# Kernel tuning notes

Measured on AMD Instinct MI355X. Metric: run time of the kernel, lower is better.

The kernel has to match this reference:

```python
import jax, jax.numpy as jnp
import numpy as np
import math

B, L, NV, PRED = 8, 512, 32, 96
D, PL, STRIDE = 128, 16, 8
E, TOPN, H = 8, 2, 512
P = (L - PL) // STRIDE + 2  # 64 patches (includes replication pad of STRIDE)
BAL_COEF, Z_COEF = 0.01, 0.001


def sinusoid_pe(n, d):
    pos = np.arange(n, dtype=np.float32)[:, None]
    div = np.exp(np.arange(0, d, 2, dtype=np.float32) * -(math.log(10000.0) / d))
    pe = np.zeros((n, d), dtype=np.float32)
    pe[:, 0::2] = np.sin(pos * div)
    pe[:, 1::2] = np.cos(pos * div)
    return jnp.asarray(pe)


def setup_inputs() -> dict:
    key = jax.random.key(0)
    ks = jax.random.split(key, 10)
    return {
        "x_enc": jax.random.normal(ks[0], (B, L, NV), jnp.float32),
        "x_mark_enc": jax.random.normal(ks[1], (B, L, 4), jnp.float32),
        "x_dec": jnp.zeros((B, 144, NV), jnp.float32),
        "x_mark_dec": jnp.zeros((B, 144, 4), jnp.float32),
        "W_patch": jax.random.normal(ks[2], (PL, D), jnp.float32) * 0.05,
        "Wg": jax.random.normal(ks[3], (D, E), jnp.float32) * 0.05,
        "W1": jax.random.normal(ks[4], (E, D, H), jnp.float32) * 0.05,
        "b1": jnp.zeros((E, H), jnp.float32),
        "W2": jax.random.normal(ks[5], (E, H, D), jnp.float32) * 0.05,
        "b2": jnp.zeros((E, D), jnp.float32),
        "W_head": jax.random.normal(ks[6], (D * P, PRED), jnp.float32) * 0.02,
        "b_head": jnp.zeros((PRED,), jnp.float32),
    }


def _forward(x_enc, W_patch, Wg, W1, b1, W2, b2, W_head, b_head):
    # instance norm over time (detached stats, like the torch code)
    means = jax.lax.stop_gradient(jnp.mean(x_enc, axis=1, keepdims=True))
    xc = x_enc - means
    stdev = jax.lax.stop_gradient(
        jnp.sqrt(jnp.mean((x_enc - means) ** 2, axis=1, keepdims=True) + 1e-5))
    xc = xc / stdev
    # [B, NV, L] -> replication pad right by STRIDE -> unfold into patches
    x = jnp.transpose(xc, (0, 2, 1))
    xp = jnp.pad(x, ((0, 0), (0, 0), (0, STRIDE)), mode="edge")
    idx = jnp.arange(P)[:, None] * STRIDE + jnp.arange(PL)[None, :]  # [P, PL]
    patches = xp[:, :, idx]  # [B, NV, P, PL]
    tok = patches.reshape(B * NV, P, PL)
    h = jnp.einsum("tpl,ld->tpd", tok, W_patch) + sinusoid_pe(P, D)[None]
    # ---- MoE over flattened tokens ----
    N = B * NV * P
    xf = h.reshape(N, D)
    logits = xf @ Wg                              # [N, E]
    probs = jax.nn.softmax(logits, axis=-1)
    gates, tops = jax.lax.top_k(probs, TOPN)      # [N, TOPN]
    # dense per-expert FFN (exact GELU, as nn.GELU default)
    eh = jax.nn.gelu(jnp.einsum("nd,edh->neh", xf, W1) + b1, approximate=False)
    eo = jnp.einsum("neh,ehd->ned", eh, W2) + b2  # [N, E, D]
    onehot = jax.nn.one_hot(tops, E, dtype=xf.dtype)          # [N, TOPN, E]
    cw = jnp.einsum("nk,nke->ne", gates, onehot)              # combine weights
    y = jnp.einsum("ne,ned->nd", cw, eo)
    # aux losses: load-balance + router z-loss
    mask = onehot.sum(axis=1)                                  # [N, E]
    balance = E * jnp.sum(jnp.mean(probs, axis=0) * jnp.mean(mask, axis=0)) / TOPN
    zloss = jnp.mean(jax.nn.logsumexp(logits, axis=-1) ** 2)
    aux = BAL_COEF * balance + Z_COEF * zloss
    # ---- head ----
    enc = y.reshape(B, NV, P, D).transpose(0, 1, 3, 2)         # [B, NV, D, P]
    flat = enc.reshape(B, NV, D * P)
    dec = flat @ W_head + b_head                               # [B, NV, PRED]
    dec = jnp.transpose(dec, (0, 2, 1))                        # [B, PRED, NV]
    dec = dec * stdev[:, 0, :][:, None, :] + means[:, 0, :][:, None, :]
    return dec, aux


def reference(x_enc, x_mark_enc, x_dec, x_mark_dec, W_patch, Wg, W1, b1, W2, b2,
              W_head, b_head):
    return _forward(x_enc, W_patch, Wg, W1, b1, W2, b2, W_head, b_head)
```

## Files before the change

kernel.cpp:

```cpp
#include <hip/hip_runtime.h>
#include <math.h>


typedef __attribute__((ext_vector_type(8))) short bf16x8;
typedef __attribute__((ext_vector_type(4))) float f32x4;

__device__ __forceinline__ float bf2f(unsigned short u){
  unsigned x = ((unsigned)u) << 16; float f; __builtin_memcpy(&f, &x, 4); return f;
}
__device__ __forceinline__ unsigned short f2bf(float f){
  unsigned x; __builtin_memcpy(&x, &f, 4);
  return (unsigned short)((x + 0x7FFFu + ((x >> 16) & 1u)) >> 16);
}
__device__ __forceinline__ float ldin(const void* p, int i, int f32){
  return f32 ? ((const float*)p)[i] : bf2f(((const unsigned short*)p)[i]);
}
__device__ __forceinline__ void stout(void* p, int i, float v, int f32){
  if (f32) ((float*)p)[i] = v; else ((unsigned short*)p)[i] = f2bf(v);
}
__device__ __forceinline__ f32x4 mfma16(bf16x8 a, bf16x8 b, f32x4 c){
  return __builtin_amdgcn_mfma_f32_16x16x32_bf16(a, b, c, 0, 0, 0);
}
#define BAR_RAW() asm volatile("s_waitcnt lgkmcnt(0)\n\ts_barrier" ::: "memory")
__device__ __forceinline__ float gelu_fast(float v){
  float u = v*v;
  float inner = v * fmaf(0.044715f, u, 1.0f);
  float e = __expf(-1.5957691216f * inner);
  return v / (1.0f + e);
}

#define OFF_SUMS   64
#define OFF_MEANS  256
#define OFF_STDS   1280
#define OFF_ECNT   2304
#define OFF_PE     3328
#define OFF_W1T    134400
#define OFF_W2T    1182976
#define OFF_WHT    2231552
#define OFF_CW     3804416
#define OFF_XFBF   4328704
#define OFF_FLATB  8523008
#define OFF_EO     12717312
#define OFF_TOKSLOT 79826176
#define OFF_DECP   79957248

__global__ __launch_bounds__(256) void k_prep_tr(const void* __restrict__ W1,
                                                 const void* __restrict__ W2,
                                                 const void* __restrict__ Wh,
                                                 int f32, float* pe,
                                                 unsigned short* W1T, unsigned short* W2T,
                                                 unsigned short* WhT){
  int t = threadIdx.x;
  if (blockIdx.x == 0){
    for (int i = t; i < 8192; i += 256){
      int p = i >> 7, d = i & 127;
      float freq = __expf(-(float)(d & ~1) * 0.07195578415606394f);
      float ang = (float)p * freq;
      pe[i] = (d & 1) ? __cosf(ang) : __sinf(ang);
    }
    return;
  }
  __shared__ float tile[32*33];
  int tb = blockIdx.x - 1;
  int r = t >> 3, cg = (t & 7) * 4;
  const void* src; unsigned short* dst;
  int in0, instride, out0, outstride;
  if (tb < 512){
    int e = tb >> 6, ti = tb & 63, d0 = (ti & 3) * 32, h0 = (ti >> 2) * 32;
    src = W1; dst = W1T;
    in0 = e*65536 + d0*512 + h0; instride = 512;
    out0 = e*65536 + h0*128 + d0; outstride = 128;
  } else if (tb < 1024){
    int tc = tb - 512;
    int e = tc >> 6, ti = tc & 63, d0 = (ti & 3) * 32, h0 = (ti >> 2) * 32;
    src = W2; dst = W2T;
    in0 = e*65536 + h0*128 + d0; instride = 128;
    out0 = e*65536 + d0*512 + h0; outstride = 512;
  } else {
    int tc = tb - 1024;
    int kt = tc / 3, nt = tc - kt*3;
    int k0 = kt*32, n0 = nt*32;
    src = Wh; dst = WhT;
    in0 = k0*96 + n0; instride = 96;
    out0 = n0*8192 + k0; outstride = 8192;
  }
  #pragma unroll
  for (int j = 0; j < 4; ++j)
    tile[r*33 + cg + j] = ldin(src, in0 + r*instride + cg + j, f32);
  __syncthreads();
  ushort4 o;
  o.x = f2bf(tile[(cg+0)*33 + r]);
  o.y = f2bf(tile[(cg+1)*33 + r]);
  o.z = f2bf(tile[(cg+2)*33 + r]);
  o.w = f2bf(tile[(cg+3)*33 + r]);
  *(ushort4*)(dst + out0 + r*outstride + cg) = o;
}

__global__ __launch_bounds__(256) void k_embed(const void* __restrict__ xe,
                                               const void* __restrict__ Wp,
                                               const void* __restrict__ Wg,
                                               int f32,
                                               const float* __restrict__ peg,
                                               float* means, float* stds,
                                               unsigned short* xfbf, float* cwg,
                                               float* sums,
                                               int* ecnt, int* elist, int* tokslot){
  __shared__ float xn[512];
  __shared__ float WpL[2048];
  __shared__ float WgL[1024];
  __shared__ float Xf[8192];
  __shared__ float lp[1024];
  __shared__ float taux[576];
  __shared__ float reds[256], redss[256];
  __shared__ float msh[2];
  __shared__ int lcnt[8], lbase[8];

  int bv = blockIdx.x;
  int b = bv >> 5, v = bv & 31;
  int t = threadIdx.x;

  if (t < 8) lcnt[t] = 0;

  float x0 = ldin(xe, (b*512 + t)*32 + v, f32);
  float x1 = ldin(xe, (b*512 + t + 256)*32 + v, f32);
  xn[t] = x0; xn[t+256] = x1;
  reds[t] = x0 + x1; redss[t] = x0*x0 + x1*x1;
  #pragma unroll
  for (int it = 0; it < 8; ++it)
    WpL[it*256 + t] = ldin(Wp, it*256 + t, f32);
  #pragma unroll
  for (int j = 0; j < 4; ++j)
    WgL[j*256 + t] = ldin(Wg, j*256 + t, f32);
  __syncthreads();
  for (int s = 128; s > 0; s >>= 1){
    if (t < s){ reds[t] += reds[t+s]; redss[t] += redss[t+s]; }
    __syncthreads();
  }
  if (t == 0){
    float m = reds[0] / 512.f;
    float sd = sqrtf(redss[0] / 512.f - m*m + 1e-5f);
    msh[0] = m; msh[1] = 1.f / sd;
    means[bv] = m; stds[bv] = sd;
  }
  __syncthreads();
  float mean = msh[0], rstd = msh[1];
  xn[t] = (xn[t] - mean) * rstd;
  xn[t+256] = (xn[t+256] - mean) * rstd;
  __syncthreads();
  {
    int p = t >> 2, q = t & 3;
    float tv[16];
    #pragma unroll
    for (int l = 0; l < 16; ++l){
      int xi = p*8 + l; if (xi > 511) xi = 511;
      tv[l] = xn[xi];
    }
    for (int dd = 0; dd < 32; ++dd){
      int d = q*32 + dd;
      float acc = peg[p*128 + d];
      #pragma unroll
      for (int l = 0; l < 16; ++l) acc += tv[l] * WpL[l*128 + d];
      Xf[p*128 + d] = acc;
    }
  }
  __syncthreads();
  if (t < 128){
    int p = t >> 1, half = t & 1;
    float s[8] = {0,0,0,0,0,0,0,0};
    for (int d = half*64; d < half*64 + 64; ++d){
      float xv = Xf[p*128 + d];
      #pragma unroll
      for (int e = 0; e < 8; ++e) s[e] += xv * WgL[d*8 + e];
    }
    #pragma unroll
    for (int e = 0; e < 8; ++e) lp[(p*2 + half)*8 + e] = s[e];
  }
  __syncthreads();
  int bi = 0, si = 0, lo0 = 0, lo1 = 0;
  if (t < 64){
    int p = t;
    float lg[8];
    #pragma unroll
    for (int e = 0; e < 8; ++e) lg[e] = lp[(p*2)*8 + e] + lp[(p*2+1)*8 + e];
    float m = lg[0];
    #pragma unroll
    for (int e = 1; e < 8; ++e) m = fmaxf(m, lg[e]);
    float pr[8]; float se = 0.f;
    #pragma unroll
    for (int e = 0; e < 8; ++e){ pr[e] = __expf(lg[e] - m); se += pr[e]; }
    float inv = 1.f / se;
    float lse = m + logf(se);
    #pragma unroll
    for (int e = 0; e < 8; ++e) pr[e] *= inv;
    float best = -1.f;
    #pragma unroll
    for (int e = 0; e < 8; ++e) if (pr[e] > best){ best = pr[e]; bi = e; }
    float sec = -1.f;
    #pragma unroll
    for (int e = 0; e < 8; ++e) if (e != bi && pr[e] > sec){ sec = pr[e]; si = e; }
    #pragma unroll
    for (int e = 0; e < 8; ++e){
      float w = (e == bi) ? best : ((e == si) ? sec : 0.f);
      cwg[(bv*64 + p)*8 + e] = w;
      taux[p*9 + e] = pr[e];
    }
    taux[p*9 + 8] = lse * lse;
    lp[p] = (float)bi; lp[64 + p] = (float)si;
    lo0 = atomicAdd(&lcnt[bi], 1);
    lo1 = atomicAdd(&lcnt[si], 1);
  }
  __syncthreads();
  if (t < 8) lbase[t] = atomicAdd(ecnt + t*32, lcnt[t]);
  __syncthreads();
  if (t < 64){
    int n = bv*64 + t;
    int p0 = lbase[bi] + lo0, p1 = lbase[si] + lo1;
    elist[bi*16384 + p0] = n;
    elist[si*16384 + p1] = n;
    tokslot[n*2]     = (bi << 14) + p0;
    tokslot[n*2 + 1] = (si << 14) + p1;
  }
  if (t < 17){
    float s = 0.f;
    if (t < 8){ for (int p = 0; p < 64; ++p) s += taux[p*9 + t]; }
    else if (t < 16){
      int e = t - 8;
      for (int p = 0; p < 64; ++p)
        s += ((int)lp[p] == e || (int)lp[64+p] == e) ? 1.f : 0.f;
    }
    else { for (int p = 0; p < 64; ++p) s += taux[p*9 + 8]; }
    atomicAdd(sums + t, s);
  }
  #pragma unroll
  for (int pass = 0; pass < 4; ++pass){
    int idx = pass*256 + t;
    int base = idx*8;
    bf16x8 o;
    #pragma unroll
    for (int j = 0; j < 8; ++j) o[j] = (short)f2bf(Xf[base + j]);
    *(bf16x8*)(xfbf + bv*8192 + base) = o;
  }
}

__global__ __launch_bounds__(256, 3) void k_moe(const unsigned short* __restrict__ xfbf,
                                                const unsigned short* __restrict__ W1T,
                                                const unsigned short* __restrict__ W2T,
                                                const void* __restrict__ b1g,
                                                int f32,
                                                const float* __restrict__ cwg,
                                                const int* __restrict__ ecnt,
                                                const int* __restrict__ elist,
                                                float* __restrict__ Eo){
  __shared__ __align__(16) char lds[49664];
  short* Xs  = (short*)(lds);
  short* Bu1 = (short*)(lds + 8704);
  short* Bu2 = (short*)(lds + 26112);
  short* Ag  = (short*)(lds + 44544);
  float* cws = (float*)(lds + 49152);
  int*   lsn = (int*)(lds + 49280);

  int t = threadIdx.x;
  int wave = t >> 6, lane = t & 63;
  int quad = lane >> 4, li = lane & 15;
  int c1 = wave * 16;
  int c2 = wave * 32;

  for (int tb = blockIdx.x; tb < 1536; tb += 768){
    int e = 8, ti = 0;
    {
      int acc = 0;
      #pragma unroll
      for (int ee = 0; ee < 8; ++ee){
        int tl = (ecnt[ee*32] + 31) >> 5;
        if (e == 8 && tb < acc + tl){ e = ee; ti = tb - acc; }
        acc += tl;
      }
    }
    if (e == 8) break;
    int cntE = ecnt[e*32];
    int tbase = ti*32;

    const unsigned short* W1e = W1T + e*65536;
    const unsigned short* W2e = W2T + e*65536;

    bf16x8 pf1[4], pf2[4];
    #pragma unroll
    for (int pass = 0; pass < 4; ++pass){
      int idx = pass*64 + lane;
      int row = idx >> 4, kg = idx & 15;
      pf1[pass] = *(const bf16x8*)(W1e + (c1 + row)*128 + kg*8);
    }
    #pragma unroll
    for (int pass = 0; pass < 4; ++pass){
      int idx = pass*64 + lane;
      int row = idx >> 3, kg = idx & 7;
      pf2[pass] = *(const bf16x8*)(W2e + (c2 + row)*512 + kg*8);
    }

    if (t < 32){
      int ok = (tbase + t) < cntE;
      int n = ok ? elist[e*16384 + tbase + t] : 0;
      lsn[t] = n;
      cws[t] = ok ? cwg[n*8 + e] : 0.f;
    }
    __syncthreads();
    #pragma unroll
    for (int pass = 0; pass < 2; ++pass){
      int idx = pass*256 + t;
      int row = idx >> 4, kg = idx & 15;
      int n = lsn[row];
      *(bf16x8*)(Xs + row*136 + kg*8) =
        *(const bf16x8*)(xfbf + n*128 + kg*8);
    }
    float cwv[2][4];
    #pragma unroll
    for (int rt = 0; rt < 2; ++rt)
      #pragma unroll
      for (int r = 0; r < 4; ++r)
        cwv[rt][r] = cws[rt*16 + quad*4 + r];
    __syncthreads();

    f32x4 Yacc[2][2];
    #pragma unroll
    for (int a = 0; a < 2; ++a)
      #pragma unroll
      for (int bb = 0; bb < 2; ++bb){ f32x4 z = {0.f,0.f,0.f,0.f}; Yacc[a][bb] = z; }

    for (int hc = 0; hc < 8; ++hc){
      #pragma unroll
      for (int pass = 0; pass < 4; ++pass){
        int idx = pass*64 + lane;
        int row = idx >> 4, kg = idx & 15;
        *(bf16x8*)(Bu1 + (c1 + row)*136 + kg*8) = pf1[pass];
      }
      #pragma unroll
      for (int pass = 0; pass < 4; ++pass){
        int idx = pass*64 + lane;
        int row = idx >> 3, kg = idx & 7;
        *(bf16x8*)(Bu2 + (c2 + row)*72 + kg*8) = pf2[pass];
      }
      float bias = ldin(b1g, e*512 + hc*64 + c1 + li, f32);
      if (hc < 7){
        #pragma unroll
        for (int pass = 0; pass < 4; ++pass){
          int idx = pass*64 + lane;
          int row = idx >> 4, kg = idx & 15;
          pf1[pass] = *(const bf16x8*)(W1e + ((hc+1)*64 + c1 + row)*128 + kg*8);
        }
        #pragma unroll
        for (int pass = 0; pass < 4; ++pass){
          int idx = pass*64 + lane;
          int row = idx >> 3, kg = idx & 7;
          pf2[pass] = *(const bf16x8*)(W2e + (c2 + row)*512 + (hc+1)*64 + kg*8);
        }
      }
      f32x4 acc1[2];
      { f32x4 z = {0.f,0.f,0.f,0.f}; acc1[0] = z; acc1[1] = z; }
      #pragma unroll
      for (int ks = 0; ks < 4; ++ks){
        int kk = ks*32 + quad*8;
        bf16x8 a0 = *(const bf16x8*)(Xs + li*136 + kk);
        bf16x8 a1 = *(const bf16x8*)(Xs + (16 + li)*136 + kk);
        bf16x8 b0 = *(const bf16x8*)(Bu1 + (c1 + li)*136 + kk);
        acc1[0] = mfma16(a0, b0, acc1[0]);
        acc1[1] = mfma16(a1, b0, acc1[1]);
      }
      BAR_RAW();
      #pragma unroll
      for (int rt = 0; rt < 2; ++rt){
        #pragma unroll
        for (int r = 0; r < 4; ++r){
          int row = rt*16 + quad*4 + r;
          float g = gelu_fast(acc1[rt][r] + bias);
          Ag[row*72 + c1 + li] = (short)f2bf(g * cwv[rt][r]);
        }
      }
      BAR_RAW();
      #pragma unroll
      for (int ks = 0; ks < 2; ++ks){
        int kk = ks*32 + quad*8;
        bf16x8 a0 = *(const bf16x8*)(Ag + li*72 + kk);
        bf16x8 a1 = *(const bf16x8*)(Ag + (16 + li)*72 + kk);
        #pragma unroll
        for (int ct = 0; ct < 2; ++ct){
          bf16x8 bb = *(const bf16x8*)(Bu2 + (c2 + ct*16 + li)*72 + kk);
          Yacc[0][ct] = mfma16(a0, bb, Yacc[0][ct]);
          Yacc[1][ct] = mfma16(a1, bb, Yacc[1][ct]);
        }
      }
    }
    #pragma unroll
    for (int ct = 0; ct < 2; ++ct){
      int col = c2 + ct*16 + li;
      #pragma unroll
      for (int rt = 0; rt < 2; ++rt)
        #pragma unroll
        for (int r = 0; r < 4; ++r){
          int row = rt*16 + quad*4 + r;
          if (tbase + row < cntE)
            Eo[(size_t)((e << 14) + tbase + row)*128 + col] = Yacc[rt][ct][r];
        }
    }
  }
}

__global__ __launch_bounds__(256) void k_flat(const float* __restrict__ Eo,
                                              const int* __restrict__ tokslot,
                                              const float* __restrict__ cwg,
                                              const void* __restrict__ b2g,
                                              int f32,
                                              unsigned short* __restrict__ flatb){
  __shared__ float Yl[64*130];
  __shared__ float b2f[1024];
  __shared__ float cwl[512];
  __shared__ int tsl[128];
  int bv = blockIdx.x;
  int t = threadIdx.x;
  if (t < 64){
    int2 v = *(const int2*)(tokslot + (bv*64 + t)*2);
    tsl[t*2] = v.x; tsl[t*2+1] = v.y;
  }
  #pragma unroll
  for (int j = 0; j < 4; ++j) b2f[j*256 + t] = ldin(b2g, j*256 + t, f32);
  #pragma unroll
  for (int j = 0; j < 2; ++j) cwl[j*256 + t] = cwg[bv*512 + j*256 + t];
  __syncthreads();
  #pragma unroll
  for (int pass = 0; pass < 32; ++pass){
    int idx = pass*256 + t;
    int row = idx >> 7, col = idx & 127;
    Yl[row*130 + col] = Eo[(size_t)tsl[row*2]*128 + col]
                      + Eo[(size_t)tsl[row*2+1]*128 + col];
  }
  __syncthreads();
  int d = t >> 1, ph = (t & 1) * 32;
  float b2c[8];
  #pragma unroll
  for (int e = 0; e < 8; ++e) b2c[e] = b2f[e*128 + d];
  unsigned short ob[32];
  for (int j = 0; j < 32; ++j){
    int p = ph + j;
    float add = 0.f;
    #pragma unroll
    for (int e = 0; e < 8; ++e) add += cwl[p*8 + e] * b2c[e];
    ob[j] = f2bf(Yl[p*130 + d] + add);
  }
  #pragma unroll
  for (int m = 0; m < 4; ++m)
    *(bf16x8*)(flatb + bv*8192 + d*64 + ph + m*8) = *(bf16x8*)(ob + m*8);
}

__global__ __launch_bounds__(256) void k_head(const unsigned short* __restrict__ flatb,
                                              const unsigned short* __restrict__ WhT,
                                              float* __restrict__ dec_part){
  int t = threadIdx.x;
  int mt = blockIdx.x & 15, kc = blockIdx.x >> 4;
  int wave = t >> 6, lane = t & 63, quad = lane >> 4, li = lane & 15;
  int kbase = kc*512 + wave*128;
  f32x4 acc[6];
  #pragma unroll
  for (int nt = 0; nt < 6; ++nt){ f32x4 z = {0.f,0.f,0.f,0.f}; acc[nt] = z; }
  #pragma unroll
  for (int ks = 0; ks < 4; ++ks){
    int k = kbase + ks*32 + quad*8;
    bf16x8 a = *(const bf16x8*)(flatb + (mt*16 + li)*8192 + k);
    #pragma unroll
    for (int nt = 0; nt < 6; ++nt){
      bf16x8 b = *(const bf16x8*)(WhT + (nt*16 + li)*8192 + k);
      acc[nt] = mfma16(a, b, acc[nt]);
    }
  }
  __shared__ float redsh[4][16][96];
  #pragma unroll
  for (int nt = 0; nt < 6; ++nt)
    #pragma unroll
    for (int r = 0; r < 4; ++r)
      redsh[wave][quad*4 + r][nt*16 + li] = acc[nt][r];
  __syncthreads();
  #pragma unroll
  for (int u = 0; u < 6; ++u){
    int o = t*6 + u;
    int row = o / 96, col = o % 96;
    float s = redsh[0][row][col] + redsh[1][row][col] + redsh[2][row][col] + redsh[3][row][col];
    dec_part[kc*24576 + (mt*16 + row)*96 + col] = s;
  }
}

__global__ __launch_bounds__(256) void k_final(const float* __restrict__ dec_part,
                                               const void* __restrict__ bh,
                                               int f32,
                                               const float* __restrict__ means,
                                               const float* __restrict__ stds,
                                               const float* __restrict__ sums,
                                               void* out){
  int o = blockIdx.x*256 + threadIdx.x;
  int b = o / 3072, rem = o % 3072, j = rem >> 5, v = rem & 31;
  int bv = b*32 + v;
  int idx = bv*96 + j;
  float s = 0.f;
  #pragma unroll
  for (int kc = 0; kc < 16; ++kc) s += dec_part[kc*24576 + idx];
  float val = (s + ldin(bh, j, f32)) * stds[bv] + means[bv];
  stout(out, o, val, f32);
  if (o == 0){
    float bal = 0.f;
    for (int e = 0; e < 8; ++e) bal += (sums[e] / 16384.f) * (sums[8+e] / 16384.f);
    bal = 8.f * bal / 2.f;
    float aux = 0.01f * bal + 0.001f * (sums[16] / 16384.f);
    stout(out, 24576, aux, f32);
  }
}

extern "C" void kernel_launch(void* const* d_in, const int* in_sizes, int n_in,
                              void* d_out, int out_size, void* d_ws, size_t ws_size,
                              hipStream_t stream){
  const void* xe = d_in[0];
  const void* Wp = d_in[4];
  const void* Wg = d_in[5];
  const void* W1 = d_in[6];
  const void* b1 = d_in[7];
  const void* W2 = d_in[8];
  const void* b2 = d_in[9];
  const void* Wh = d_in[10];
  const void* bh = d_in[11];

  int f32 = 1;
  if (in_sizes && n_in > 0 && in_sizes[0] == 262144) f32 = 0;

  char* ws = (char*)d_ws;
  float* sums  = (float*)(ws + OFF_SUMS);
  float* means = (float*)(ws + OFF_MEANS);
  float* stds  = (float*)(ws + OFF_STDS);
  int*   ecnt  = (int*)(ws + OFF_ECNT);
  float* pe    = (float*)(ws + OFF_PE);
  unsigned short* W1T   = (unsigned short*)(ws + OFF_W1T);
  unsigned short* W2T   = (unsigned short*)(ws + OFF_W2T);
  unsigned short* WhT   = (unsigned short*)(ws + OFF_WHT);
  float* cw    = (float*)(ws + OFF_CW);
  unsigned short* xfbf  = (unsigned short*)(ws + OFF_XFBF);
  unsigned short* flatb = (unsigned short*)(ws + OFF_FLATB);
  int*   elist = (int*)(ws + OFF_FLATB);
  float* Eo    = (float*)(ws + OFF_EO);
  int*   tokslot = (int*)(ws + OFF_TOKSLOT);
  float* dec_part = (float*)(ws + OFF_DECP);

  hipMemsetAsync(ws, 0, 3328, stream);
  k_prep_tr<<<1793, 256, 0, stream>>>(W1, W2, Wh, f32, pe, W1T, W2T, WhT);
  k_embed<<<256, 256, 0, stream>>>(xe, Wp, Wg, f32, pe, means, stds,
                                   xfbf, cw, sums, ecnt, elist, tokslot);
  k_moe<<<768, 256, 0, stream>>>(xfbf, W1T, W2T, b1, f32, cw, ecnt, elist, Eo);
  k_flat<<<256, 256, 0, stream>>>(Eo, tokslot, cw, b2, f32, flatb);
  k_head<<<256, 256, 0, stream>>>(flatb, WhT, dec_part);
  k_final<<<96, 256, 0, stream>>>(dec_part, bh, f32, means, stds, sums, d_out);
}
```

Baseline: 157.3 us.

## Merge weight-transpose and embed kernels; compute PE inline; double-buffer MoE activation tile

Fuses the weight transpose/convert kernel and the embedding/routing kernel into one launch: blocks below 256 do the embed work and the rest do the transposes. The positional encoding is now computed inline instead of being read from a precomputed buffer. In the MoE kernel the GELU activation tile is double-buffered across hidden chunks, which removes one barrier per chunk, and two __syncthreads are replaced with raw barriers. This removes a launch and some synchronisation, but raises the fused kernel's LDS use, which may lower occupancy for the transpose blocks, and adds transcendental math to the embed blocks.

```diff
diff --git a/kernel.cpp b/kernel.cpp
--- a/kernel.cpp
+++ b/kernel.cpp
@@ -33,7 +33,6 @@
 #define OFF_MEANS  256
 #define OFF_STDS   1280
 #define OFF_ECNT   2304
-#define OFF_PE     3328
 #define OFF_W1T    134400
 #define OFF_W2T    1182976
 #define OFF_WHT    2231552
@@ -44,80 +43,74 @@
 #define OFF_TOKSLOT 79826176
 #define OFF_DECP   79957248
 
-__global__ __launch_bounds__(256) void k_prep_tr(const void* __restrict__ W1,
-                                                 const void* __restrict__ W2,
-                                                 const void* __restrict__ Wh,
-                                                 int f32, float* pe,
-                                                 unsigned short* W1T, unsigned short* W2T,
-                                                 unsigned short* WhT){
+__global__ __launch_bounds__(256) void k_prep(const void* __restrict__ xe,
+                                              const void* __restrict__ Wp,
+                                              const void* __restrict__ Wg,
+                                              const void* __restrict__ W1,
+                                              const void* __restrict__ W2,
+                                              const void* __restrict__ Wh,
+                                              int f32,
+                                              float* means, float* stds,
+                                              unsigned short* xfbf, float* cwg,
+                                              float* sums,
+                                              int* ecnt, int* elist, int* tokslot,
+                                              unsigned short* W1T, unsigned short* W2T,
+                                              unsigned short* WhT){
+  __shared__ __align__(16) char sh[55680];
   int t = threadIdx.x;
-  if (blockIdx.x == 0){
-    for (int i = t; i < 8192; i += 256){
-      int p = i >> 7, d = i & 127;
-      float freq = __expf(-(float)(d & ~1) * 0.07195578415606394f);
-      float ang = (float)p * freq;
-      pe[i] = (d & 1) ? __cosf(ang) : __sinf(ang);
-    }
+
+  if (blockIdx.x >= 256){
+    float* tile = (float*)sh;
+    int tb = blockIdx.x - 256;
+    int r = t >> 3, cg = (t & 7) * 4;
+    const void* src; unsigned short* dst;
+    int in0, instride, out0, outstride;
+    if (tb < 512){
+      int e = tb >> 6, ti = tb & 63, d0 = (ti & 3) * 32, h0 = (ti >> 2) * 32;
+      src = W1; dst = W1T;
+      in0 = e*65536 + d0*512 + h0; instride = 512;
+      out0 = e*65536 + h0*128 + d0; outstride = 128;
+    } else if (tb < 1024){
+      int tc = tb - 512;
+      int e = tc >> 6, ti = tc & 63, d0 = (ti & 3) * 32, h0 = (ti >> 2) * 32;
+      src = W2; dst = W2T;
+      in0 = e*65536 + h0*128 + d0; instride = 128;
+      out0 = e*65536 + d0*512 + h0; outstride = 512;
+    } else {
+      int tc = tb - 1024;
+      int kt = tc / 3, nt = tc - kt*3;
+      int k0 = kt*32, n0 = nt*32;
+      src = Wh; dst = WhT;
+      in0 = k0*96 + n0; instride = 96;
+      out0 = n0*8192 + k0; outstride = 8192;
+    }
+    #pragma unroll
+    for (int j = 0; j < 4; ++j)
+      tile[r*33 + cg + j] = ldin(src, in0 + r*instride + cg + j, f32);
+    __syncthreads();
+    ushort4 o;
+    o.x = f2bf(tile[(cg+0)*33 + r]);
+    o.y = f2bf(tile[(cg+1)*33 + r]);
+    o.z = f2bf(tile[(cg+2)*33 + r]);
+    o.w = f2bf(tile[(cg+3)*33 + r]);
+    *(ushort4*)(dst + out0 + r*outstride + cg) = o;
     return;
   }
-  __shared__ float tile[32*33];
-  int tb = blockIdx.x - 1;
-  int r = t >> 3, cg = (t & 7) * 4;
-  const void* src; unsigned short* dst;
-  int in0, instride, out0, outstride;
-  if (tb < 512){
-    int e = tb >> 6, ti = tb & 63, d0 = (ti & 3) * 32, h0 = (ti >> 2) * 32;
-    src = W1; dst = W1T;
-    in0 = e*65536 + d0*512 + h0; instride = 512;
-    out0 = e*65536 + h0*128 + d0; outstride = 128;
-  } else if (tb < 1024){
-    int tc = tb - 512;
-    int e = tc >> 6, ti = tc & 63, d0 = (ti & 3) * 32, h0 = (ti >> 2) * 32;
-    src = W2; dst = W2T;
-    in0 = e*65536 + h0*128 + d0; instride = 128;
-    out0 = e*65536 + d0*512 + h0; outstride = 512;
-  } else {
-    int tc = tb - 1024;
-    int kt = tc / 3, nt = tc - kt*3;
-    int k0 = kt*32, n0 = nt*32;
-    src = Wh; dst = WhT;
-    in0 = k0*96 + n0; instride = 96;
-    out0 = n0*8192 + k0; outstride = 8192;
-  }
-  #pragma unroll
-  for (int j = 0; j < 4; ++j)
-    tile[r*33 + cg + j] = ldin(src, in0 + r*instride + cg + j, f32);
-  __syncthreads();
-  ushort4 o;
-  o.x = f2bf(tile[(cg+0)*33 + r]);
-  o.y = f2bf(tile[(cg+1)*33 + r]);
-  o.z = f2bf(tile[(cg+2)*33 + r]);
-  o.w = f2bf(tile[(cg+3)*33 + r]);
-  *(ushort4*)(dst + out0 + r*outstride + cg) = o;
-}
-
-__global__ __launch_bounds__(256) void k_embed(const void* __restrict__ xe,
-                                               const void* __restrict__ Wp,
-                                               const void* __restrict__ Wg,
-                                               int f32,
-                                               const float* __restrict__ peg,
-                                               float* means, float* stds,
-                                               unsigned short* xfbf, float* cwg,
-                                               float* sums,
-                                               int* ecnt, int* elist, int* tokslot){
-  __shared__ float xn[512];
-  __shared__ float WpL[2048];
-  __shared__ float WgL[1024];
-  __shared__ float Xf[8192];
-  __shared__ float lp[1024];
-  __shared__ float taux[576];
-  __shared__ float reds[256], redss[256];
-  __shared__ float msh[2];
-  __shared__ int lcnt[8], lbase[8];
+
+  float* xn    = (float*)(sh);
+  float* WpL   = (float*)(sh + 2048);
+  float* WgL   = (float*)(sh + 10240);
+  float* Xf    = (float*)(sh + 14336);
+  float* lp    = (float*)(sh + 47104);
+  float* taux  = (float*)(sh + 51200);
+  float* reds  = (float*)(sh + 53504);
+  float* redss = (float*)(sh + 54528);
+  float* msh   = (float*)(sh + 55552);
+  int*   lcnt  = (int*)(sh + 55560);
+  int*   lbase = (int*)(sh + 55592);
 
   int bv = blockIdx.x;
   int b = bv >> 5, v = bv & 31;
-  int t = threadIdx.x;
 
   if (t < 8) lcnt[t] = 0;
 
@@ -157,7 +150,9 @@
     }
     for (int dd = 0; dd < 32; ++dd){
       int d = q*32 + dd;
-      float acc = peg[p*128 + d];
+      float freq = __expf(-(float)(d & ~1) * 0.07195578415606394f);
+      float ang = (float)p * freq;
+      float acc = (d & 1) ? __cosf(ang) : __sinf(ang);
       #pragma unroll
       for (int l = 0; l < 16; ++l) acc += tv[l] * WpL[l*128 + d];
       Xf[p*128 + d] = acc;
@@ -251,13 +246,14 @@
                                                 const int* __restrict__ ecnt,
                                                 const int* __restrict__ elist,
                                                 float* __restrict__ Eo){
-  __shared__ __align__(16) char lds[49664];
+  __shared__ __align__(16) char lds[54016];
   short* Xs  = (short*)(lds);
   short* Bu1 = (short*)(lds + 8704);
   short* Bu2 = (short*)(lds + 26112);
-  short* Ag  = (short*)(lds + 44544);
-  float* cws = (float*)(lds + 49152);
-  int*   lsn = (int*)(lds + 49280);
+  short* Ag0 = (short*)(lds + 44544);
+  short* Ag1 = (short*)(lds + 49152);
+  float* cws = (float*)(lds + 53760);
+  int*   lsn = (int*)(lds + 53888);
 
   int t = threadIdx.x;
   int wave = t >> 6, lane = t & 63;
@@ -303,7 +299,7 @@
       lsn[t] = n;
       cws[t] = ok ? cwg[n*8 + e] : 0.f;
     }
-    __syncthreads();
+    BAR_RAW();
     #pragma unroll
     for (int pass = 0; pass < 2; ++pass){
       int idx = pass*256 + t;
@@ -318,7 +314,7 @@
       #pragma unroll
       for (int r = 0; r < 4; ++r)
         cwv[rt][r] = cws[rt*16 + quad*4 + r];
-    __syncthreads();
+    BAR_RAW();
 
     f32x4 Yacc[2][2];
     #pragma unroll
@@ -327,6 +323,7 @@
       for (int bb = 0; bb < 2; ++bb){ f32x4 z = {0.f,0.f,0.f,0.f}; Yacc[a][bb] = z; }
 
     for (int hc = 0; hc < 8; ++hc){
+      short* Agc = (hc & 1) ? Ag1 : Ag0;
       #pragma unroll
       for (int pass = 0; pass < 4; ++pass){
         int idx = pass*64 + lane;
@@ -365,22 +362,21 @@
         acc1[0] = mfma16(a0, b0, acc1[0]);
         acc1[1] = mfma16(a1, b0, acc1[1]);
       }
-      BAR_RAW();
       #pragma unroll
       for (int rt = 0; rt < 2; ++rt){
         #pragma unroll
         for (int r = 0; r < 4; ++r){
           int row = rt*16 + quad*4 + r;
           float g = gelu_fast(acc1[rt][r] + bias);
-          Ag[row*72 + c1 + li] = (short)f2bf(g * cwv[rt][r]);
+          Agc[row*72 + c1 + li] = (short)f2bf(g * cwv[rt][r]);
         }
       }
       BAR_RAW();
       #pragma unroll
       for (int ks = 0; ks < 2; ++ks){
         int kk = ks*32 + quad*8;
-        bf16x8 a0 = *(const bf16x8*)(Ag + li*72 + kk);
-        bf16x8 a1 = *(const bf16x8*)(Ag + (16 + li)*72 + kk);
+        bf16x8 a0 = *(const bf16x8*)(Agc + li*72 + kk);
+        bf16x8 a1 = *(const bf16x8*)(Agc + (16 + li)*72 + kk);
         #pragma unroll
         for (int ct = 0; ct < 2; ++ct){
           bf16x8 bb = *(const bf16x8*)(Bu2 + (c2 + ct*16 + li)*72 + kk);
@@ -532,7 +528,6 @@
   float* means = (float*)(ws + OFF_MEANS);
   float* stds  = (float*)(ws + OFF_STDS);
   int*   ecnt  = (int*)(ws + OFF_ECNT);
-  float* pe    = (float*)(ws + OFF_PE);
   unsigned short* W1T   = (unsigned short*)(ws + OFF_W1T);
   unsigned short* W2T   = (unsigned short*)(ws + OFF_W2T);
   unsigned short* WhT   = (unsigned short*)(ws + OFF_WHT);
@@ -545,9 +540,9 @@
   float* dec_part = (float*)(ws + OFF_DECP);
 
   hipMemsetAsync(ws, 0, 3328, stream);
-  k_prep_tr<<<1793, 256, 0, stream>>>(W1, W2, Wh, f32, pe, W1T, W2T, WhT);
-  k_embed<<<256, 256, 0, stream>>>(xe, Wp, Wg, f32, pe, means, stds,
-                                   xfbf, cw, sums, ecnt, elist, tokslot);
+  k_prep<<<2048, 256, 0, stream>>>(xe, Wp, Wg, W1, W2, Wh, f32,
+                                   means, stds, xfbf, cw, sums,
+                                   ecnt, elist, tokslot, W1T, W2T, WhT);
   k_moe<<<768, 256, 0, stream>>>(xfbf, W1T, W2T, b1, f32, cw, ecnt, elist, Eo);
   k_flat<<<256, 256, 0, stream>>>(Eo, tokslot, cw, b2, f32, flatb);
   k_head<<<256, 256, 0, stream>>>(flatb, WhT, dec_part);
```

Measured after the change: 162.7 us. 1.03x slower.
